# Kernel tuning notes

Hardware: AMD Instinct MI355X
Metric: run time of the kernel (lower is better)

## Reference

```python
import jax, jax.numpy as jnp
import numpy as np

R_MIN, R_MAX, THETA_MAX = 0.4, 0.99, 6.283185307179586
ORDER = 64  # K = order//2 = 32 pole pairs


def setup_inputs() -> dict:
    key = jax.random.key(0)
    k1, k2, k3, k4, k5 = jax.random.split(key, 5)
    K, D = ORDER // 2, 1024
    u1 = jax.random.uniform(k1, (K, D), dtype=jnp.float32)
    u2 = jax.random.uniform(k2, (K, D), dtype=jnp.float32)
    scale = np.sqrt(2.0 / ORDER).astype(np.float32)
    return {
        "r": R_MIN + (R_MAX - R_MIN) * u1,                         # pole radii
        "theta": THETA_MAX * u2,                                    # pole angles
        "R_re": jax.random.normal(k3, (K, D), dtype=jnp.float32) * scale,
        "R_im": jax.random.normal(k4, (K, D), dtype=jnp.float32) * scale,
        "h_0": jax.random.normal(k5, (1, D), dtype=jnp.float32),
        "L": 2048,
    }


def reference(r, theta, R_re, R_im, h_0, L):
    # poles p = r * exp(i*theta), residues R = R_re + i*R_im; shapes (K, D)
    p = r.astype(jnp.complex64) * jnp.exp(1j * theta.astype(jnp.complex64))
    R = R_re + 1j * R_im                                            # (K, D) complex64
    t = jnp.arange(L - 1, dtype=jnp.float32)[:, None, None]         # (L-1, 1, 1)
    # h[t, d] = Re( sum_k R[k,d] * p[k,d]^t )
    h = jnp.sum(R[None] * p[None] ** t, axis=1).real                # (L-1, D)
    h = jnp.concatenate([h_0, h], axis=0)                           # (L, D)
    return h.T                                                      # (D, L)
```

## Files before the change

### kernel.cpp

```cpp
#include <hip/hip_runtime.h>


#define KP 32
#define DD 1024
#define LL 2048

__global__ __launch_bounds__(256) void modal_filter_kernel(
    const float* __restrict__ r, const float* __restrict__ theta,
    const float* __restrict__ Rre, const float* __restrict__ Rim,
    const float* __restrict__ h0, float* __restrict__ out) {
  const int d = blockIdx.x;
  const int tid = threadIdx.x;

  __shared__ float s_lr[KP];
  __shared__ float s_th[KP];
  __shared__ float s_Rre[KP];
  __shared__ float s_Rim[KP];
  if (tid < KP) {
    s_lr[tid]  = __logf(r[tid * DD + d]);
    s_th[tid]  = theta[tid * DD + d];
    s_Rre[tid] = Rre[tid * DD + d];
    s_Rim[tid] = Rim[tid * DD + d];
  }
  __syncthreads();

  float* outd = out + (size_t)d * LL;

  for (int l = tid; l < LL; l += 256) {
    float acc;
    if (l == 0) {
      acc = h0[d];
    } else {
      const float t = (float)(l - 1);
      acc = 0.0f;
#pragma unroll
      for (int k = 0; k < KP; ++k) {
        const float mag = __expf(t * s_lr[k]);
        float s, c;
        __sincosf(t * s_th[k], &s, &c);
        acc = fmaf(mag, fmaf(s_Rre[k], c, -(s_Rim[k] * s)), acc);
      }
    }
    outd[l] = acc;
  }
}

extern "C" void kernel_launch(void* const* d_in, const int* in_sizes, int n_in,
                              void* d_out, int out_size, void* d_ws, size_t ws_size,
                              hipStream_t stream) {
  const float* r     = (const float*)d_in[0];
  const float* theta = (const float*)d_in[1];
  const float* Rre   = (const float*)d_in[2];
  const float* Rim   = (const float*)d_in[3];
  const float* h0    = (const float*)d_in[4];
  float* out = (float*)d_out;

  modal_filter_kernel<<<DD, 256, 0, stream>>>(r, theta, Rre, Rim, h0, out);
}
```

Before: 89.80 us.

## Replace per-sample exp/sincos with complex rotation recurrence across strided samples

After: 80.04 us. 1.12x faster.

```diff
diff --git a/kernel.cpp b/kernel.cpp
--- a/kernel.cpp
+++ b/kernel.cpp
@@ -4,6 +4,7 @@
 #define KP 32
 #define DD 1024
 #define LL 2048
+#define INV_2PI 0x1.45f306p-3f
 
 __global__ __launch_bounds__(256) void modal_filter_kernel(
     const float* __restrict__ r, const float* __restrict__ theta,
@@ -13,35 +14,68 @@
   const int tid = threadIdx.x;
 
   __shared__ float s_lr[KP];
-  __shared__ float s_th[KP];
+  __shared__ float s_thr[KP];
+  __shared__ float s_qre[KP];
+  __shared__ float s_qim[KP];
   __shared__ float s_Rre[KP];
   __shared__ float s_Rim[KP];
+
   if (tid < KP) {
-    s_lr[tid]  = __logf(r[tid * DD + d]);
-    s_th[tid]  = theta[tid * DD + d];
+    const float rv = r[tid * DD + d];
+    const float th = theta[tid * DD + d];
+    const float lr = __builtin_amdgcn_logf(rv);
+    const float thr = th * INV_2PI;
+    const float qmag = __builtin_amdgcn_exp2f(256.0f * lr);
+    const float qang = __builtin_amdgcn_fractf(256.0f * thr);
+    s_lr[tid] = lr;
+    s_thr[tid] = thr;
+    s_qre[tid] = qmag * __builtin_amdgcn_cosf(qang);
+    s_qim[tid] = qmag * __builtin_amdgcn_sinf(qang);
     s_Rre[tid] = Rre[tid * DD + d];
     s_Rim[tid] = Rim[tid * DD + d];
   }
   __syncthreads();
 
+  float zre[KP], zim[KP], qre[KP], qim[KP];
+  const float t0 = (float)tid - 1.0f;
+#pragma unroll
+  for (int k = 0; k < KP; ++k) {
+    const float mag = __builtin_amdgcn_exp2f(t0 * s_lr[k]);
+    const float ang = __builtin_amdgcn_fractf(t0 * s_thr[k]);
+    const float c = __builtin_amdgcn_cosf(ang);
+    const float s = __builtin_amdgcn_sinf(ang);
+    const float wre = mag * c, wim = mag * s;
+    zre[k] = s_Rre[k] * wre - s_Rim[k] * wim;
+    zim[k] = s_Rre[k] * wim + s_Rim[k] * wre;
+    qre[k] = s_qre[k];
+    qim[k] = s_qim[k];
+  }
+
   float* outd = out + (size_t)d * LL;
+  const float h0d = h0[d];
 
-  for (int l = tid; l < LL; l += 256) {
-    float acc;
-    if (l == 0) {
-      acc = h0[d];
-    } else {
-      const float t = (float)(l - 1);
-      acc = 0.0f;
+#pragma unroll
+  for (int s = 0; s < 8; ++s) {
+    float a0 = 0.f, a1 = 0.f, a2 = 0.f, a3 = 0.f;
+#pragma unroll
+    for (int k = 0; k < KP; k += 4) {
+      a0 += zre[k];
+      a1 += zre[k + 1];
+      a2 += zre[k + 2];
+      a3 += zre[k + 3];
+    }
+    const float acc = (a0 + a1) + (a2 + a3);
+    const int l = tid + 256 * s;
+    outd[l] = (l == 0) ? h0d : acc;
+    if (s < 7) {
 #pragma unroll
       for (int k = 0; k < KP; ++k) {
-        const float mag = __expf(t * s_lr[k]);
-        float s, c;
-        __sincosf(t * s_th[k], &s, &c);
-        acc = fmaf(mag, fmaf(s_Rre[k], c, -(s_Rim[k] * s)), acc);
+        const float nr = zre[k] * qre[k] - zim[k] * qim[k];
+        const float ni = zre[k] * qim[k] + zim[k] * qre[k];
+        zre[k] = nr;
+        zim[k] = ni;
       }
     }
-    outd[l] = acc;
   }
 }
 
```
